# Performance work log

Measured on AMD Instinct MI355X. Metric: run time of the kernel, lower is better.

The kernel has to match this reference:

```python
import jax, jax.numpy as jnp
import numpy as np

FEAT_RES = 512
FEAT_DIM = 48
WIDTH = 128
IN_DIM = FEAT_DIM + 27 + 63  # 138
N_RAYS, N_SAMPLES = 4096, 128


def positional_encode(x, L):
    freqs = (2.0 ** jnp.arange(L)).astype(x.dtype)            # [L]
    xf = x[..., None, :] * freqs[:, None]                      # [..., L, 3]
    enc = jnp.concatenate([jnp.sin(xf), jnp.cos(xf)], axis=-1) # [..., L, 6]
    return jnp.concatenate([x, enc.reshape(x.shape[:-1] + (L * 6,))], axis=-1)


def grid_sample_bilinear(plane, gx, gy):
    # plane: [C, H, W]; gx, gy: [N, S] in [-1, 1]; align_corners=True, zeros padding
    H, W = plane.shape[-2], plane.shape[-1]
    ix = (gx + 1.0) * 0.5 * (W - 1)
    iy = (gy + 1.0) * 0.5 * (H - 1)
    x0 = jnp.floor(ix); y0 = jnp.floor(iy)
    x1 = x0 + 1.0;      y1 = y0 + 1.0
    wx1 = ix - x0; wx0 = 1.0 - wx1
    wy1 = iy - y0; wy0 = 1.0 - wy1

    def gather(xi, yi, w):
        valid = (xi >= 0) & (xi <= W - 1) & (yi >= 0) & (yi <= H - 1)
        xc = jnp.clip(xi, 0, W - 1).astype(jnp.int32)
        yc = jnp.clip(yi, 0, H - 1).astype(jnp.int32)
        v = plane[:, yc, xc]                                   # [C, N, S]
        return v * (w * valid.astype(w.dtype))[None]

    return (gather(x0, y0, wx0 * wy0) + gather(x1, y0, wx1 * wy0)
            + gather(x0, y1, wx0 * wy1) + gather(x1, y1, wx1 * wy1))


def setup_inputs() -> dict:
    key = jax.random.key(0)
    ks = jax.random.split(key, 12)
    x = jax.random.uniform(ks[0], (N_RAYS, N_SAMPLES, 3), jnp.float32, -3.0, 3.0)
    d = jax.random.normal(ks[1], (N_RAYS, 3), jnp.float32)
    d = d / jnp.linalg.norm(d, axis=-1, keepdims=True)
    feat = jax.random.normal(ks[2], (3, FEAT_DIM, FEAT_RES, FEAT_RES), jnp.float32)
    s = 0.05
    W0 = jax.random.normal(ks[3], (IN_DIM, WIDTH), jnp.float32) * s
    b0 = jnp.zeros((WIDTH,), jnp.float32)
    W1 = jax.random.normal(ks[4], (WIDTH, WIDTH), jnp.float32) * s
    b1 = jnp.zeros((WIDTH,), jnp.float32)
    W2 = jax.random.normal(ks[5], (WIDTH, WIDTH), jnp.float32) * s
    b2 = jnp.zeros((WIDTH,), jnp.float32)
    W3 = jax.random.normal(ks[6], (WIDTH, 4), jnp.float32) * s
    b3 = jnp.zeros((4,), jnp.float32)
    return {"x": x, "d": d, "feat": feat, "W0": W0, "b0": b0,
            "W1": W1, "b1": b1, "W2": W2, "b2": b2, "W3": W3, "b3": b3}


def reference(x, d, feat, W0, b0, W1, b1, W2, b2, W3, b3):
    x = x / 3.0                                                # [N, S, 3]
    f_xy = grid_sample_bilinear(feat[0], x[..., 0], x[..., 1])  # [C, N, S]
    f_yz = grid_sample_bilinear(feat[1], x[..., 1], x[..., 2])
    f_xz = grid_sample_bilinear(feat[2], x[..., 0], x[..., 2])
    f_sum = jnp.moveaxis(f_xy + f_yz + f_xz, 0, -1)            # [N, S, C]

    d_rep = jnp.broadcast_to(d[:, None, :], x.shape)           # [N, S, 3]
    h = jnp.concatenate([f_sum, positional_encode(d_rep, 4), positional_encode(x, 10)], axis=-1)

    h = jax.nn.relu(h @ W0 + b0)
    h = jax.nn.relu(h @ W1 + b1)
    h = jax.nn.relu(h @ W2 + b2)
    out = h @ W3 + b3                                          # [N, S, 4]
    return jnp.concatenate([out[..., :3], jax.nn.relu(out[..., 3:])], axis=-1)
```

## Files before the change

### kernel.cpp

```cpp
#include <hip/hip_runtime.h>
#include <hip/hip_bf16.h>
#include <hip/hip_fp16.h>
#include <cstdint>
#include <cstddef>

#define NPLANE 262144
#define HSTR 144
#define PW_LAYER 18432
#define NCELL 32768
#define NSAMP 524288
#define NRAY 4096

#define WS_FEAT_OFF 131072
#define FEAT_BYTES  75497472
#define WS_CNT_OFF  (WS_FEAT_OFF + FEAT_BYTES)
#define WS_OFFS_OFF (WS_CNT_OFF + 131072)
#define WS_XS_OFF   (WS_OFFS_OFF + 131072)
#define WS_PED_OFF  (WS_XS_OFF + (size_t)NSAMP*16)
#define WS_END      (WS_PED_OFF + (size_t)NRAY*28*2)

#define TRS_BLKS 3072
#define PREP_BLKS 216
#define PED_BLKS 16
#define SCAT_BLKS 2048
#define K2_BLKS (TRS_BLKS + PREP_BLKS + PED_BLKS + SCAT_BLKS)

typedef unsigned int uint;
typedef __attribute__((ext_vector_type(16))) float f32x16;
typedef _Float16 half8 __attribute__((ext_vector_type(8)));

__device__ __forceinline__ unsigned short f16u(float f){
    __half h = __float2half(f);
    return *reinterpret_cast<unsigned short*>(&h);
}
__device__ __forceinline__ f32x16 mfma16_(half8 a, half8 b, f32x16 c){
    return __builtin_amdgcn_mfma_f32_32x32x16_f16(a, b, c, 0,0,0);
}

__device__ __forceinline__ uint part3(uint v){
    v &= 0x3ff;
    v = (v | (v<<16)) & 0x030000FFu;
    v = (v | (v<<8))  & 0x0300F00Fu;
    v = (v | (v<<4))  & 0x030C30C3u;
    v = (v | (v<<2))  & 0x09249249u;
    return v;
}
__device__ __forceinline__ uint cellkey(float x0, float x1, float x2){
    const float s = 1.0f/3.0f;
    const int cx = min(max((int)((x0*s+1.0f)*16.0f),0),31);
    const int cy = min(max((int)((x1*s+1.0f)*16.0f),0),31);
    const int cz = min(max((int)((x2*s+1.0f)*16.0f),0),31);
    return part3((uint)cx) | (part3((uint)cy)<<1) | (part3((uint)cz)<<2);
}

__global__ __launch_bounds__(256) void hist_k(const float* __restrict__ x, uint* __restrict__ counts){
    const int i = blockIdx.x*256 + threadIdx.x;
    if (i >= NSAMP) return;
    atomicAdd(&counts[cellkey(x[3*i], x[3*i+1], x[3*i+2])], 1u);
}

__global__ __launch_bounds__(1024) void scan_k(const uint* __restrict__ counts, uint* __restrict__ offs){
    __shared__ uint ps[1024];
    const int t = threadIdx.x;
    uint loc[32]; uint s = 0;
    #pragma unroll
    for (int i=0;i<32;++i){ loc[i] = counts[t*32+i]; s += loc[i]; }
    ps[t] = s; __syncthreads();
    for (int off=1; off<1024; off<<=1){
        uint v = (t>=off) ? ps[t-off] : 0u;
        __syncthreads();
        ps[t] += v;
        __syncthreads();
    }
    uint base = ps[t] - s;
    #pragma unroll
    for (int i=0;i<32;++i){ offs[t*32+i] = base; base += loc[i]; }
}

__global__ __launch_bounds__(256) void prepass_k(const float* __restrict__ feat,
                                                 const float* __restrict__ W0,
                                                 const float* __restrict__ W1,
                                                 const float* __restrict__ W2,
                                                 const float* __restrict__ b0,
                                                 const float* __restrict__ b1,
                                                 const float* __restrict__ b2,
                                                 const float* __restrict__ d,
                                                 const float* __restrict__ x,
                                                 uint* __restrict__ offs,
                                                 unsigned short* __restrict__ featT,
                                                 unsigned short* __restrict__ wp,
                                                 unsigned short* __restrict__ ped,
                                                 float4* __restrict__ xs){
    const int bid = blockIdx.x, tid = threadIdx.x;
    if (bid < TRS_BLKS){
        __shared__ unsigned short lb[256*50];
        const int pos = bid*256 + tid;
        const int p  = pos >> 18;
        const int yx = pos & (NPLANE-1);
        const float* src = feat + (size_t)p*48*NPLANE + yx;
        #pragma unroll 4
        for (int c = 0; c < 48; ++c){
            lb[tid*50 + c] = f16u(src[(size_t)c*NPLANE]);
        }
        __syncthreads();
        uint4* dst = (uint4*)(featT + (size_t)bid*(256*48));
        #pragma unroll
        for (int m = 0; m < 6; ++m){
            const int u4 = tid + m*256;
            const int byteoff = u4*16;
            const int smp = byteoff/96;
            const int off = (byteoff%96) >> 2;
            const uint* rw = (const uint*)(lb + smp*50);
            uint4 val; val.x = rw[off]; val.y = rw[off+1]; val.z = rw[off+2]; val.w = rw[off+3];
            dst[u4] = val;
        }
        return;
    }
    if (bid < TRS_BLKS + PREP_BLKS){
        const int idx = (bid - TRS_BLKS)*256 + tid;
        if (idx >= 3*PW_LAYER) return;
        const int L = idx / PW_LAYER, base = idx % PW_LAYER;
        const float* W = (L==0)? W0 : (L==1)? W1 : W2;
        const float* B = (L==0)? b0 : (L==1)? b1 : b2;
        const int KREAL = (L==0)? 138 : 128;
        const int e  = base & 7;
        const int l  = (base >> 3) & 63;
        const int fr = base >> 9;
        const int ks = fr >> 2, nt = fr & 3;
        const int k  = ks*16 + (l >> 5)*8 + e;
        const int n  = nt*32 + (l & 31);
        float v = 0.f;
        if (k < KREAL) v = W[k*128 + n];
        else if (k == KREAL) v = B[n];
        wp[idx] = f16u(v);
        return;
    }
    if (bid < TRS_BLKS + PREP_BLKS + PED_BLKS){
        const int ray = (bid - TRS_BLKS - PREP_BLKS)*256 + tid;
        if (ray >= NRAY) return;
        const float dv0 = d[ray*3], dv1 = d[ray*3+1], dv2 = d[ray*3+2];
        unsigned short* row = ped + ray*28;
        row[0]=f16u(dv0); row[1]=f16u(dv1); row[2]=f16u(dv2);
        #pragma unroll
        for (int l=0;l<4;++l){
            const float sc = (float)(1<<l);
            float sv, cv;
            __sincosf(dv0*sc, &sv, &cv); row[3+l*6+0]=f16u(sv); row[3+l*6+3]=f16u(cv);
            __sincosf(dv1*sc, &sv, &cv); row[3+l*6+1]=f16u(sv); row[3+l*6+4]=f16u(cv);
            __sincosf(dv2*sc, &sv, &cv); row[3+l*6+2]=f16u(sv); row[3+l*6+5]=f16u(cv);
        }
        row[27] = 0;
        return;
    }
    {
        const int i = (bid - TRS_BLKS - PREP_BLKS - PED_BLKS)*256 + tid;
        if (i >= NSAMP) return;
        const float x0 = x[3*i], x1 = x[3*i+1], x2 = x[3*i+2];
        const uint pos = atomicAdd(&offs[cellkey(x0,x1,x2)], 1u);
        xs[pos] = make_float4(x0, x1, x2, __int_as_float(i));
    }
}

__device__ __forceinline__ void run_layer(unsigned short* Hw, const unsigned short* __restrict__ Wp,
                                          int lane, int ln31, int kg, const int* pr){
    const unsigned short* Hrow = Hw + ln31*HSTR;
    f32x16 acc[4];
    #pragma unroll
    for (int i=0;i<4;++i) acc[i] = (f32x16)0.f;
    #pragma unroll
    for (int h=0; h<2; ++h){
        half8 bf[10];
        #pragma unroll
        for (int i=0;i<10;++i){
            const int ks = i>>1, nt = 2*h + (i&1);
            bf[i] = *reinterpret_cast<const half8*>(Wp + (((ks*4+nt)*64 + lane) << 3));
        }
        #pragma unroll
        for (int ks=0; ks<5; ++ks){
            const half8 a = *reinterpret_cast<const half8*>(Hrow + ks*16 + kg*8);
            acc[2*h]   = mfma16_(a, bf[2*ks],   acc[2*h]);
            acc[2*h+1] = mfma16_(a, bf[2*ks+1], acc[2*h+1]);
        }
        #pragma unroll
        for (int i=0;i<8;++i){
            const int ks = 5 + (i>>1), nt = 2*h + (i&1);
            bf[i] = *reinterpret_cast<const half8*>(Wp + (((ks*4+nt)*64 + lane) << 3));
        }
        #pragma unroll
        for (int ks=5; ks<9; ++ks){
            const half8 a = *reinterpret_cast<const half8*>(Hrow + ks*16 + kg*8);
            acc[2*h]   = mfma16_(a, bf[2*(ks-5)],   acc[2*h]);
            acc[2*h+1] = mfma16_(a, bf[2*(ks-5)+1], acc[2*h+1]);
        }
    }
    #pragma unroll
    for (int nt=0;nt<4;++nt){
        #pragma unroll
        for (int r=0;r<16;++r){
            const int row = pr[r] >> 8;
            const int col = nt*32 + (pr[r] & 255);
            Hw[row*HSTR + col] = f16u(fmaxf(acc[nt][r], 0.f));
        }
    }
}

__global__ __launch_bounds__(128, 4) void nerf_mfma(
    const unsigned short* __restrict__ featT,
    const unsigned short* __restrict__ wp0, const unsigned short* __restrict__ wp1,
    const unsigned short* __restrict__ wp2,
    const float* __restrict__ W3, const float* __restrict__ b3,
    const float4* __restrict__ xs, const unsigned short* __restrict__ ped,
    float* __restrict__ out)
{
    __shared__ unsigned short H[64*HSTR];
    __shared__ uint sW3u[256];
    __shared__ float4 sX[64];

    const int tid  = threadIdx.x;
    const int wid  = tid >> 6, lane = tid & 63;
    const int ln31 = lane & 31, kg = lane >> 5;
    const int sbase = wid * 32;
    const int base = (((int)blockIdx.x & 7)*1024 + ((int)blockIdx.x >> 3))*64 + sbase;
    unsigned short* Hw = H + sbase*HSTR;

    half8 pa = (half8)0, pb = (half8)0, qa = (half8)0, qb = (half8)0;
    if (kg == 0){
        pa[0] = (_Float16)(float)ln31;
        pb[0] = (_Float16)1.0f;
        qa[0] = (_Float16)1.0f;
        qb[0] = (_Float16)(float)ln31;
    }
    const f32x16 zz = (f32x16)0.f;
    const f32x16 D1 = mfma16_(pa, pb, zz);
    const f32x16 D2 = mfma16_(qa, qb, zz);
    int pr[16];
    #pragma unroll
    for (int r=0;r<16;++r) pr[r] = (((int)D1[r]) << 8) | (int)D2[r];

    if (lane < 32) sX[sbase + lane] = xs[base + lane];
    #pragma unroll
    for (int j=0;j<2;++j){
        const int idx = lane*2 + j;
        const int i2 = wid*128 + idx;
        const int k = i2 >> 1, c = i2 & 1;
        sW3u[i2] = ((uint)f16u(W3[k*4 + 2*c])) | (((uint)f16u(W3[k*4 + 2*c + 1])) << 16);
    }

    #pragma unroll
    for (int rr=0; rr<2; ++rr){
        if (rr == 1 && lane >= 32) break;
        const int s32 = rr ? lane : ln31;
        const int m   = rr ? 2 : kg;
        const float4 xr = sX[sbase + s32];
        const float xn = ((m==0)? xr.x : (m==1)? xr.y : xr.z) * (1.0f/3.0f);
        unsigned short* row = H + (sbase+s32)*HSTR;
        row[75+m] = f16u(xn);
        float sv, cv;
        __sincosf(xn, &sv, &cv);
        #pragma unroll
        for (int l=0;l<10;++l){
            row[78+l*6+m]   = f16u(sv);
            row[78+l*6+3+m] = f16u(cv);
            const float s2v = 2.0f*sv*cv;
            const float c2v = 1.0f - 2.0f*sv*sv;
            sv = s2v; cv = c2v;
        }
    }

    {
        const int s32 = lane >> 1, hf = lane & 1;
        const int sid = __float_as_int(sX[sbase + s32].w);
        const uint* src = (const uint*)(ped + (sid >> 7)*28) + hf*7;
        uint* dstu = (uint*)(H + (sbase+s32)*HSTR + 48) + hf*7;
        if (hf == 0){
            #pragma unroll
            for (int i=0;i<7;++i) dstu[i] = src[i];
        } else {
            #pragma unroll
            for (int i=0;i<6;++i) dstu[i] = src[i];
            H[(sbase+s32)*HSTR + 74] = ((const unsigned short*)src)[12];
        }
    }

    if (lane < 32){
        *(uint*)(H + (sbase+lane)*HSTR + 138)  = 0x00003C00u;
        *(uint2*)(H + (sbase+lane)*HSTR + 140) = make_uint2(0u, 0u);
    }

    #pragma unroll
    for (int rr=0; rr<3; ++rr){
        const int u = rr*64 + lane;
        const int s32 = u/6, ch = u - s32*6;
        const float4 xr = sX[sbase + s32];
        const float xn0 = xr.x*(1.0f/3.0f);
        const float xn1 = xr.y*(1.0f/3.0f);
        const float xn2 = xr.z*(1.0f/3.0f);
        const int c0 = ch*8;
        __half2 acc[4];
        #pragma unroll
        for (int q=0;q<4;++q) acc[q] = __float2half2_rn(0.f);
        #pragma unroll
        for (int p=0;p<3;++p){
            const float gx = (p==1)? xn1 : xn0;
            const float gy = (p==0)? xn1 : xn2;
            const float ix = ((gx+1.0f)*0.5f)*511.0f;
            const float iy = ((gy+1.0f)*0.5f)*511.0f;
            const float fx0 = floorf(ix), fy0 = floorf(iy);
            const float wx1 = ix - fx0, wy1 = iy - fy0;
            const float wx0 = 1.0f-wx1, wy0 = 1.0f-wy1;
            const int x0i = (int)fx0, y0i = (int)fy0;
            const int x0c = min(max(x0i,0),511),   x1c = min(max(x0i+1,0),511);
            const int y0c = min(max(y0i,0),511),   y1c = min(max(y0i+1,0),511);
            const uint r0 = (uint)(p*NPLANE + y0c*512);
            const uint r1 = (uint)(p*NPLANE + y1c*512);
            const uint  av[4] = {(r0+x0c)*48u, (r0+x1c)*48u, (r1+x0c)*48u, (r1+x1c)*48u};
            const float wv[4] = {wx0*wy0, wx1*wy0, wx0*wy1, wx1*wy1};
            #pragma unroll
            for (int cr=0;cr<4;++cr){
                const uint4 uv = *(const uint4*)(featT + av[cr] + c0);
                const __half2 w2 = __float2half2_rn(wv[cr]);
                union { uint4 v; __half2 h[4]; } t; t.v = uv;
                acc[0] = __hfma2(t.h[0], w2, acc[0]);
                acc[1] = __hfma2(t.h[1], w2, acc[1]);
                acc[2] = __hfma2(t.h[2], w2, acc[2]);
                acc[3] = __hfma2(t.h[3], w2, acc[3]);
            }
        }
        union { __half2 h[4]; uint4 v; } pk;
        #pragma unroll
        for (int q=0;q<4;++q) pk.h[q] = acc[q];
        *(uint4*)(H + (sbase+s32)*HSTR + c0) = pk.v;
    }

    run_layer(Hw, wp0, lane, ln31, kg, pr);
    if (lane < 32) *(uint4*)(Hw + lane*HSTR + 128) = make_uint4(0x00003C00u,0u,0u,0u);
    else           *(uint4*)(Hw + ln31*HSTR + 136) = make_uint4(0u,0u,0u,0u);
    run_layer(Hw, wp1, lane, ln31, kg, pr);
    run_layer(Hw, wp2, lane, ln31, kg, pr);

    {
        const int s32 = lane >> 1, cp = lane & 1;
        const unsigned short* hrow = Hw + s32*HSTR;
        const int sid = __float_as_int(sX[sbase + s32].w);
        const int jp = 2*cp;
        const float2 b3v = *(const float2*)(b3 + jp);
        float a0 = b3v.x, a1 = b3v.y;
        #pragma unroll
        for (int q=0;q<16;++q){
            union { uint4 v; __half2 h[4]; } u;
            u.v = *(const uint4*)(hrow + q*8);
            const int k = q*8;
            #pragma unroll
            for (int j2=0;j2<4;++j2){
                const float2 f = __half22float2(u.h[j2]);
                const int k2 = k + j2*2;
                union { uint u32; __half2 h; } w0c, w1c;
                w0c.u32 = sW3u[(k2+0)*2+cp];
                w1c.u32 = sW3u[(k2+1)*2+cp];
                const float2 w0f = __half22float2(w0c.h);
                const float2 w1f = __half22float2(w1c.h);
                a0 += f.x*w0f.x + f.y*w1f.x;
                a1 += f.x*w0f.y + f.y*w1f.y;
            }
        }
        if (cp == 1) a1 = fmaxf(a1, 0.f);
        float2 o; o.x = a0; o.y = a1;
        *(float2*)(out + (size_t)sid*4 + jp) = o;
    }
}

#define STR 148
#define SBLK 64
template<int K4, int KTAIL>
__device__ __forceinline__ void mlp_layer_fb(float (*Hs)[STR], const float* __restrict__ W,
                                             const float* __restrict__ B, int tid){
    const int tx = tid & 31, ty = tid >> 5;
    const int s0 = ty*8, j0 = tx*4;
    float acc[8][4];
    #pragma unroll
    for (int i=0;i<8;++i){ acc[i][0]=0.f; acc[i][1]=0.f; acc[i][2]=0.f; acc[i][3]=0.f; }
    for (int kk = 0; kk < K4; ++kk){
        const int k = kk*4;
        const float4 wa = *(const float4*)(W + (size_t)(k+0)*128 + j0);
        const float4 wb = *(const float4*)(W + (size_t)(k+1)*128 + j0);
        const float4 wc = *(const float4*)(W + (size_t)(k+2)*128 + j0);
        const float4 wd = *(const float4*)(W + (size_t)(k+3)*128 + j0);
        #pragma unroll
        for (int i=0;i<8;++i){
            const float4 h = *(const float4*)&Hs[s0+i][k];
            acc[i][0] += h.x*wa.x + h.y*wb.x + h.z*wc.x + h.w*wd.x;
            acc[i][1] += h.x*wa.y + h.y*wb.y + h.z*wc.y + h.w*wd.y;
            acc[i][2] += h.x*wa.z + h.y*wb.z + h.z*wc.z + h.w*wd.z;
            acc[i][3] += h.x*wa.w + h.y*wb.w + h.z*wc.w + h.w*wd.w;
        }
    }
    #pragma unroll
    for (int t=0;t<KTAIL;++t){
        const int k = K4*4+t;
        const float4 wa = *(const float4*)(W + (size_t)k*128 + j0);
        #pragma unroll
        for (int i=0;i<8;++i){
            const float h = Hs[s0+i][k];
            acc[i][0] += h*wa.x; acc[i][1] += h*wa.y; acc[i][2] += h*wa.z; acc[i][3] += h*wa.w;
        }
    }
    const float4 bb = *(const float4*)(B + j0);
    __syncthreads();
    #pragma unroll
    for (int i=0;i<8;++i){
        float4 o;
        o.x = fmaxf(acc[i][0]+bb.x, 0.f);
        o.y = fmaxf(acc[i][1]+bb.y, 0.f);
        o.z = fmaxf(acc[i][2]+bb.z, 0.f);
        o.w = fmaxf(acc[i][3]+bb.w, 0.f);
        *(float4*)&Hs[s0+i][j0] = o;
    }
    __syncthreads();
}

__global__ __launch_bounds__(256) void nerf_fused_fb(
    const float* __restrict__ x, const float* __restrict__ d,
    const float* __restrict__ feat,
    const float* __restrict__ W0, const float* __restrict__ b0,
    const float* __restrict__ W1, const float* __restrict__ b1,
    const float* __restrict__ W2, const float* __restrict__ b2,
    const float* __restrict__ W3, const float* __restrict__ b3,
    float* __restrict__ out)
{
    __shared__ float Hs[SBLK][STR];
    __shared__ uint4  sA[3][SBLK];
    __shared__ float4 sW[3][SBLK];

    const int tid = threadIdx.x;
    const int g0 = blockIdx.x * SBLK;

    if (tid < 192){
        const int s = tid & 63, p = tid >> 6;
        const int g = g0 + s;
        const float xn0 = x[3*g+0]/3.0f, xn1 = x[3*g+1]/3.0f, xn2 = x[3*g+2]/3.0f;
        const float gx = (p==1)? xn1 : xn0;
        const float gy = (p==0)? xn1 : xn2;
        const float ix = ((gx+1.0f)*0.5f)*511.0f;
        const float iy = ((gy+1.0f)*0.5f)*511.0f;
        const float fx0 = floorf(ix), fy0 = floorf(iy);
        const float wx1 = ix - fx0, wy1 = iy - fy0;
        const float wx0 = 1.0f-wx1, wy0 = 1.0f-wy1;
        const int x0i = (int)fx0, y0i = (int)fy0;
        const int x0c = min(max(x0i,0),511),   x1c = min(max(x0i+1,0),511);
        const int y0c = min(max(y0i,0),511),   y1c = min(max(y0i+1,0),511);
        const uint bp = (uint)p*48u*NPLANE;
        sA[p][s] = make_uint4(bp + y0c*512 + x0c, bp + y0c*512 + x1c,
                              bp + y1c*512 + x0c, bp + y1c*512 + x1c);
        sW[p][s] = make_float4(wx0*wy0, wx1*wy0, wx0*wy1, wx1*wy1);
    }
    if (tid < 64){
        const int s = tid, g = g0 + s;
        float xn[3];
        xn[0]=x[3*g+0]/3.0f; xn[1]=x[3*g+1]/3.0f; xn[2]=x[3*g+2]/3.0f;
        Hs[s][75]=xn[0]; Hs[s][76]=xn[1]; Hs[s][77]=xn[2];
        float f = 1.0f;
        for (int l=0;l<10;++l){
            #pragma unroll
            for (int m=0;m<3;++m){
                const float a = xn[m]*f;
                Hs[s][78+l*6+m]   = sinf(a);
                Hs[s][78+l*6+3+m] = cosf(a);
            }
            f *= 2.0f;
        }
    } else if (tid < 91){
        const int k = tid-64;
        const int ray = g0 >> 7;
        float v;
        if (k < 3) v = d[ray*3+k];
        else {
            const int l=(k-3)/6, r=(k-3)%6;
            const float a = d[ray*3 + (r%3)] * (float)(1<<l);
            v = (r<3)? sinf(a) : cosf(a);
        }
        for (int s2=0;s2<64;++s2) Hs[s2][48+k]=v;
    }
    __syncthreads();

    for (int it = tid; it < 384; it += 256){
        const int s = it & 63;
        const int c0 = (it >> 6)*8;
        float acc[8];
        #pragma unroll
        for (int q=0;q<8;++q) acc[q]=0.f;
        #pragma unroll
        for (int p=0;p<3;++p){
            const uint4  aa = sA[p][s];
            const float4 ww = sW[p][s];
            const uint  av[4] = {aa.x,aa.y,aa.z,aa.w};
            const float wv[4] = {ww.x,ww.y,ww.z,ww.w};
            #pragma unroll
            for (int cr=0;cr<4;++cr){
                const float w = wv[cr];
                const float* bsrc = feat + av[cr] + (size_t)c0*NPLANE;
                #pragma unroll
                for (int q=0;q<8;++q) acc[q] += w*bsrc[(size_t)q*NPLANE];
            }
        }
        *(float4*)&Hs[s][c0]   = make_float4(acc[0],acc[1],acc[2],acc[3]);
        *(float4*)&Hs[s][c0+4] = make_float4(acc[4],acc[5],acc[6],acc[7]);
    }
    __syncthreads();

    mlp_layer_fb<34,2>(Hs, W0, b0, tid);
    mlp_layer_fb<32,0>(Hs, W1, b1, tid);
    mlp_layer_fb<32,0>(Hs, W2, b2, tid);

    {
        const int s = tid>>2, j = tid&3;
        float acc = 0.f;
        for (int kk=0; kk<32; ++kk){
            const float4 h = *(const float4*)&Hs[s][kk*4];
            const int k = kk*4;
            acc += h.x*W3[(k+0)*4+j] + h.y*W3[(k+1)*4+j]
                 + h.z*W3[(k+2)*4+j] + h.w*W3[(k+3)*4+j];
        }
        acc += b3[j];
        if (j==3) acc = fmaxf(acc, 0.f);
        out[(size_t)blockIdx.x*256 + tid] = acc;
    }
}

extern "C" void kernel_launch(void* const* d_in, const int* in_sizes, int n_in,
                              void* d_out, int out_size, void* d_ws, size_t ws_size,
                              hipStream_t stream){
    (void)in_sizes; (void)n_in; (void)out_size;
    const float* x    = (const float*)d_in[0];
    const float* ddir = (const float*)d_in[1];
    const float* feat = (const float*)d_in[2];
    const float* W0 = (const float*)d_in[3];  const float* b0 = (const float*)d_in[4];
    const float* W1 = (const float*)d_in[5];  const float* b1 = (const float*)d_in[6];
    const float* W2 = (const float*)d_in[7];  const float* b2 = (const float*)d_in[8];
    const float* W3 = (const float*)d_in[9];  const float* b3 = (const float*)d_in[10];
    float* out = (float*)d_out;

    char* wsb = (char*)d_ws;

    if (ws_size >= WS_END){
        unsigned short* wsu   = (unsigned short*)wsb;
        unsigned short* featT = (unsigned short*)(wsb + WS_FEAT_OFF);
        uint*   counts = (uint*)(wsb + WS_CNT_OFF);
        uint*   offs   = (uint*)(wsb + WS_OFFS_OFF);
        float4* xsrec  = (float4*)(wsb + WS_XS_OFF);
        unsigned short* ped = (unsigned short*)(wsb + WS_PED_OFF);
        hipMemsetAsync(counts, 0, NCELL*sizeof(uint), stream);
        hist_k<<<2048, 256, 0, stream>>>(x, counts);
        scan_k<<<1, 1024, 0, stream>>>(counts, offs);
        prepass_k<<<K2_BLKS, 256, 0, stream>>>(feat, W0, W1, W2, b0, b1, b2, ddir, x,
                                               offs, featT, wsu, ped, xsrec);
        nerf_mfma<<<8192, 128, 0, stream>>>(featT,
                                            wsu, wsu + PW_LAYER, wsu + 2*PW_LAYER,
                                            W3, b3, xsrec, ped, out);
    } else {
        nerf_fused_fb<<<8192, 256, 0, stream>>>(x, ddir, feat,
                                                W0,b0,W1,b1,W2,b2,W3,b3, out);
    }
}
```

Measured before the change: 266.5 us.

## Split MLP layers across waves by output columns instead of sample rows

```diff
diff --git a/kernel.cpp b/kernel.cpp
--- a/kernel.cpp
+++ b/kernel.cpp
@@ -161,47 +161,57 @@
     }
 }
 
-__device__ __forceinline__ void run_layer(unsigned short* Hw, const unsigned short* __restrict__ Wp,
-                                          int lane, int ln31, int kg, const int* pr){
-    const unsigned short* Hrow = Hw + ln31*HSTR;
-    f32x16 acc[4];
-    #pragma unroll
-    for (int i=0;i<4;++i) acc[i] = (f32x16)0.f;
-    #pragma unroll
-    for (int h=0; h<2; ++h){
+__device__ __forceinline__ void run_layer_ns(unsigned short* H, const unsigned short* __restrict__ Wp,
+                                             int lane, int ln31, int kg, int wid, const int* pr){
+    const unsigned short* Hrow0 = H + ln31*HSTR;
+    const unsigned short* Hrow1 = H + (32+ln31)*HSTR;
+    const int ntb = 2*wid;
+    f32x16 acc00=(f32x16)0.f, acc01=(f32x16)0.f, acc10=(f32x16)0.f, acc11=(f32x16)0.f;
+    {
         half8 bf[10];
         #pragma unroll
         for (int i=0;i<10;++i){
-            const int ks = i>>1, nt = 2*h + (i&1);
+            const int ks = i>>1, nt = ntb + (i&1);
             bf[i] = *reinterpret_cast<const half8*>(Wp + (((ks*4+nt)*64 + lane) << 3));
         }
         #pragma unroll
         for (int ks=0; ks<5; ++ks){
-            const half8 a = *reinterpret_cast<const half8*>(Hrow + ks*16 + kg*8);
-            acc[2*h]   = mfma16_(a, bf[2*ks],   acc[2*h]);
-            acc[2*h+1] = mfma16_(a, bf[2*ks+1], acc[2*h+1]);
-        }
+            const half8 a0 = *reinterpret_cast<const half8*>(Hrow0 + ks*16 + kg*8);
+            const half8 a1 = *reinterpret_cast<const half8*>(Hrow1 + ks*16 + kg*8);
+            acc00 = mfma16_(a0, bf[2*ks],   acc00);
+            acc01 = mfma16_(a0, bf[2*ks+1], acc01);
+            acc10 = mfma16_(a1, bf[2*ks],   acc10);
+            acc11 = mfma16_(a1, bf[2*ks+1], acc11);
+        }
+    }
+    {
+        half8 bf[8];
         #pragma unroll
         for (int i=0;i<8;++i){
-            const int ks = 5 + (i>>1), nt = 2*h + (i&1);
+            const int ks = 5 + (i>>1), nt = ntb + (i&1);
             bf[i] = *reinterpret_cast<const half8*>(Wp + (((ks*4+nt)*64 + lane) << 3));
         }
         #pragma unroll
         for (int ks=5; ks<9; ++ks){
-            const half8 a = *reinterpret_cast<const half8*>(Hrow + ks*16 + kg*8);
-            acc[2*h]   = mfma16_(a, bf[2*(ks-5)],   acc[2*h]);
-            acc[2*h+1] = mfma16_(a, bf[2*(ks-5)+1], acc[2*h+1]);
-        }
-    }
-    #pragma unroll
-    for (int nt=0;nt<4;++nt){
-        #pragma unroll
-        for (int r=0;r<16;++r){
-            const int row = pr[r] >> 8;
-            const int col = nt*32 + (pr[r] & 255);
-            Hw[row*HSTR + col] = f16u(fmaxf(acc[nt][r], 0.f));
-        }
-    }
+            const half8 a0 = *reinterpret_cast<const half8*>(Hrow0 + ks*16 + kg*8);
+            const half8 a1 = *reinterpret_cast<const half8*>(Hrow1 + ks*16 + kg*8);
+            acc00 = mfma16_(a0, bf[2*(ks-5)],   acc00);
+            acc01 = mfma16_(a0, bf[2*(ks-5)+1], acc01);
+            acc10 = mfma16_(a1, bf[2*(ks-5)],   acc10);
+            acc11 = mfma16_(a1, bf[2*(ks-5)+1], acc11);
+        }
+    }
+    __syncthreads();
+    #pragma unroll
+    for (int r=0;r<16;++r){
+        const int row = pr[r] >> 8;
+        const int col = ntb*32 + (pr[r] & 255);
+        H[row*HSTR + col]           = f16u(fmaxf(acc00[r], 0.f));
+        H[row*HSTR + col + 32]      = f16u(fmaxf(acc01[r], 0.f));
+        H[(row+32)*HSTR + col]      = f16u(fmaxf(acc10[r], 0.f));
+        H[(row+32)*HSTR + col + 32] = f16u(fmaxf(acc11[r], 0.f));
+    }
+    __syncthreads();
 }
 
 __global__ __launch_bounds__(128, 4) void nerf_mfma(
@@ -331,12 +341,17 @@
         for (int q=0;q<4;++q) pk.h[q] = acc[q];
         *(uint4*)(H + (sbase+s32)*HSTR + c0) = pk.v;
     }
-
-    run_layer(Hw, wp0, lane, ln31, kg, pr);
-    if (lane < 32) *(uint4*)(Hw + lane*HSTR + 128) = make_uint4(0x00003C00u,0u,0u,0u);
-    else           *(uint4*)(Hw + ln31*HSTR + 136) = make_uint4(0u,0u,0u,0u);
-    run_layer(Hw, wp1, lane, ln31, kg, pr);
-    run_layer(Hw, wp2, lane, ln31, kg, pr);
+    __syncthreads();
+
+    run_layer_ns(H, wp0, lane, ln31, kg, wid, pr);
+    {
+        const int row = tid & 63, hf = tid >> 6;
+        if (hf == 0) *(uint4*)(H + row*HSTR + 128) = make_uint4(0x00003C00u,0u,0u,0u);
+        else         *(uint4*)(H + row*HSTR + 136) = make_uint4(0u,0u,0u,0u);
+    }
+    __syncthreads();
+    run_layer_ns(H, wp1, lane, ln31, kg, wid, pr);
+    run_layer_ns(H, wp2, lane, ln31, kg, wid, pr);
 
     {
         const int s32 = lane >> 1, cp = lane & 1;
```

Result: faster. 255.4 us (-4.2%).
